# Kernel tuning notes

Hardware: AMD Instinct MI355X
Metric: run time of the kernel (lower is better)

## Reference

```python
import jax, jax.numpy as jnp
import numpy as np

HEADS = 8
D_MODEL = 512
HEAD_DIM = D_MODEL // HEADS


def setup_inputs() -> dict:
    key = jax.random.key(0)
    ks = jax.random.split(key, 13)
    B, S, D = 8, 1024, D_MODEL
    scale = 1.0 / np.sqrt(D)
    x = jax.random.normal(ks[0], (B, S, D), dtype=jnp.float32)
    names = ['cq', 'ck', 'cv', 'pq', 'pk', 'pv']
    inp = {'x': x}
    for i, n in enumerate(names):
        inp['W_' + n] = jax.random.normal(ks[1 + 2 * i], (D, D), dtype=jnp.float32) * scale
        inp['b_' + n] = jax.random.normal(ks[2 + 2 * i], (D,), dtype=jnp.float32) * 0.01
    return inp


def reference(x, W_cq, b_cq, W_ck, b_ck, W_cv, b_cv, W_pq, b_pq, W_pk, b_pk, W_pv, b_pv):
    # x: [N, S, D]. Fused common + personal QKV: (x@Wc + bc) + (x@Wp + bp)
    N, S, D = x.shape
    q = x @ (W_cq + W_pq) + (b_cq + b_pq)  # [N, S, D]
    k = x @ (W_ck + W_pk) + (b_ck + b_pk)
    v = x @ (W_cv + W_pv) + (b_cv + b_pv)
    q = q.reshape(N, S, HEADS, HEAD_DIM)
    k = k.reshape(N, S, HEADS, HEAD_DIM)
    v = v.reshape(N, S, HEADS, HEAD_DIM)
    # NOTE: original scales by sqrt(d_model), not sqrt(head_dim)
    energy = jnp.einsum('nqhd,nkhd->nhqk', q, k) / jnp.sqrt(jnp.asarray(D, x.dtype))
    attn = jax.nn.softmax(energy, axis=-1)  # [N, H, Q, K]
    out = jnp.einsum('nhqk,nkhd->nqhd', attn, v).reshape(N, S, D)
    return out
```

## Files before the change

### kernel.cpp

```cpp
#include <hip/hip_runtime.h>

#define B_   8
#define S_   1024
#define D_   512
#define H_   8
#define HD_  64
#define NT_  (B_ * S_)
#define QSCALE_ 0.06376387f
#define C4_    5.7707802f

typedef _Float16 f16;
typedef _Float16 f16x4 __attribute__((ext_vector_type(4)));
typedef _Float16 f16x8 __attribute__((ext_vector_type(8)));
typedef float    f32x4 __attribute__((ext_vector_type(4)));

#define GLOAD_LDS16(g, l) \
    __builtin_amdgcn_global_load_lds( \
        (const __attribute__((address_space(1))) unsigned int*)(g), \
        (__attribute__((address_space(3))) unsigned int*)(l), 16, 0, 0)

#define MFMA16(a, b, c) __builtin_amdgcn_mfma_f32_16x16x32_f16(a, b, c, 0, 0, 0)

__global__ __launch_bounds__(256) void prep_fused(
    const float* __restrict__ x, f16* __restrict__ xh,
    const float* __restrict__ Wcq, const float* __restrict__ Wck, const float* __restrict__ Wcv,
    const float* __restrict__ Wpq, const float* __restrict__ Wpk, const float* __restrict__ Wpv,
    f16* __restrict__ Bt)
{
    __shared__ float tile[64][68];
    const int tid = threadIdx.x;

    if (blockIdx.x < 2048) {
        int i = (blockIdx.x * 256 + tid) * 8;
        float4 a = *(const float4*)(x + i);
        float4 b = *(const float4*)(x + i + 4);
        f16x8 o = { (f16)a.x, (f16)a.y, (f16)a.z, (f16)a.w,
                    (f16)b.x, (f16)b.y, (f16)b.z, (f16)b.w };
        *(f16x8*)(xh + i) = o;
        return;
    }

    const int wk = blockIdx.x - 2048;
    const int k0 = (wk & 7) * 64;
    const int n0 = (wk >> 3) * 64;
    const int g  = n0 >> 9;
    const int c0 = n0 & 511;
    const float* Wc = (g == 0) ? Wcq : (g == 1) ? Wck : Wcv;
    const float* Wp = (g == 0) ? Wpq : (g == 1) ? Wpk : Wpv;

#pragma unroll
    for (int it = 0; it < 4; ++it) {
        int row = it * 16 + (tid >> 4);
        int c4  = (tid & 15) * 4;
        float4 a = *(const float4*)(Wc + (size_t)(k0 + row) * D_ + c0 + c4);
        float4 b = *(const float4*)(Wp + (size_t)(k0 + row) * D_ + c0 + c4);
        tile[row][c4 + 0] = a.x + b.x;
        tile[row][c4 + 1] = a.y + b.y;
        tile[row][c4 + 2] = a.z + b.z;
        tile[row][c4 + 3] = a.w + b.w;
    }
    __syncthreads();
#pragma unroll
    for (int it = 0; it < 2; ++it) {
        int nr = it * 32 + (tid >> 3);
        int kc = (tid & 7) * 8;
        f16x8 o;
#pragma unroll
        for (int j = 0; j < 8; ++j) o[j] = (f16)tile[kc + j][nr];
        *(f16x8*)(Bt + (size_t)(n0 + nr) * D_ + k0 + kc) = o;
    }
}

__global__ __launch_bounds__(256) void qkv_gemm(
    const f16* __restrict__ xh, const f16* __restrict__ Bt,
    const float* __restrict__ bcq, const float* __restrict__ bck, const float* __restrict__ bcv,
    const float* __restrict__ bpq, const float* __restrict__ bpk, const float* __restrict__ bpv,
    f16* __restrict__ Qh, f16* __restrict__ Kws, f16* __restrict__ Vws)
{
    __shared__ __align__(16) char smem_raw[36864];

    const int m0 = blockIdx.x * 128;
    const int n0 = blockIdx.y * 128;
    const int tid  = threadIdx.x;
    const int lane = tid & 63;
    const int wave = tid >> 6;
    const int wr = wave >> 1, wc = wave & 1;
    const int lo4 = lane & 15, hi4 = lane >> 4;

    const int r0 = tid >> 2;
    const int w0 = tid & 3;
    const f16* gA  = xh + (size_t)(m0 + r0) * D_ + w0 * 8;
    const f16* gA2 = xh + (size_t)(m0 + r0 + 64) * D_ + w0 * 8;
    const f16* gB  = Bt + (size_t)(n0 + r0) * D_ + w0 * 8;
    const f16* gB2 = Bt + (size_t)(n0 + r0 + 64) * D_ + w0 * 8;
    const int dA  = tid * 8;
    const int dA2 = (tid + 256) * 8;

#define STAGE(bufsel, kt) do { \
        f16* _A = (f16*)(smem_raw + (bufsel) * 16384); \
        f16* _B = (f16*)(smem_raw + (bufsel) * 16384 + 8192); \
        GLOAD_LDS16(gA  + (kt) * 32, _A + dA);  \
        GLOAD_LDS16(gA2 + (kt) * 32, _A + dA2); \
        GLOAD_LDS16(gB  + (kt) * 32, _B + dA);  \
        GLOAD_LDS16(gB2 + (kt) * 32, _B + dA2); \
    } while (0)

    f32x4 acc[4][4];
#pragma unroll
    for (int i = 0; i < 4; ++i)
#pragma unroll
        for (int j = 0; j < 4; ++j) acc[i][j] = (f32x4){0.f, 0.f, 0.f, 0.f};

    STAGE(0, 0);
    asm volatile("s_waitcnt vmcnt(0)" ::: "memory");
    __syncthreads();

    for (int t = 0; t < 16; ++t) {
        const int cur = t & 1;
        if (t < 15) STAGE(cur ^ 1, t + 1);

        const f16* Ab = (const f16*)(smem_raw + cur * 16384);
        const f16* Bb = (const f16*)(smem_raw + cur * 16384 + 8192);
        f16x8 a[4], b[4];
#pragma unroll
        for (int i = 0; i < 4; ++i)
            a[i] = *(const f16x8*)(Ab + (wr * 64 + i * 16 + lo4) * 32 + hi4 * 8);
#pragma unroll
        for (int j = 0; j < 4; ++j)
            b[j] = *(const f16x8*)(Bb + (wc * 64 + j * 16 + lo4) * 32 + hi4 * 8);
#pragma unroll
        for (int i = 0; i < 4; ++i)
#pragma unroll
            for (int j = 0; j < 4; ++j)
                acc[i][j] = MFMA16(a[i], b[j], acc[i][j]);

        asm volatile("s_waitcnt vmcnt(0)" ::: "memory");
        __syncthreads();
    }
#undef STAGE

    const int g = n0 >> 9;
    const float* bc = (g == 0) ? bcq : (g == 1) ? bck : bcv;
    const float* bp = (g == 0) ? bpq : (g == 1) ? bpk : bpv;

    const int colb = n0 + wc * 64;
    const int h    = (colb & 511) >> 6;
    const int rowb = m0 + wr * 64;
    const int bb   = rowb >> 10;
    const int s0   = rowb & 1023;

    float bias[4];
#pragma unroll
    for (int j = 0; j < 4; ++j) {
        const int cg = (colb + j * 16 + lo4) & 511;
        bias[j] = bc[cg] + bp[cg];
    }

    f16* Cs = (f16*)smem_raw + wave * 4608;
    const size_t bhbase = (size_t)(bb * H_ + h) * 65536;

    if (g == 2) {
#pragma unroll
        for (int i = 0; i < 4; ++i)
#pragma unroll
            for (int j = 0; j < 4; ++j) {
                f16x4 v = { (f16)(acc[i][j][0] + bias[j]), (f16)(acc[i][j][1] + bias[j]),
                            (f16)(acc[i][j][2] + bias[j]), (f16)(acc[i][j][3] + bias[j]) };
                *(f16x4*)(Cs + (j * 16 + lo4) * 72 + i * 16 + hi4 * 4) = v;
            }
        asm volatile("s_waitcnt lgkmcnt(0)" ::: "memory");
        __builtin_amdgcn_sched_barrier(0);
        const size_t tbase = bhbase + (size_t)(s0 >> 6) * 4096;
#pragma unroll
        for (int it = 0; it < 8; ++it) {
            const int d  = it * 8 + (lane >> 3);
            const int cs = lane & 7;
            f16x8 chunk = *(const f16x8*)(Cs + d * 72 + cs * 8);
            *(f16x8*)(Vws + tbase + d * 64 + ((cs ^ (d & 7)) << 3)) = chunk;
        }
    } else {
        const float scale = (g == 0) ? QSCALE_ : 1.f;
#pragma unroll
        for (int i = 0; i < 4; ++i)
#pragma unroll
            for (int j = 0; j < 4; ++j)
#pragma unroll
                for (int r = 0; r < 4; ++r)
                    Cs[(i * 16 + hi4 * 4 + r) * 72 + j * 16 + lo4] =
                        (f16)((acc[i][j][r] + bias[j]) * scale);
        asm volatile("s_waitcnt lgkmcnt(0)" ::: "memory");
        __builtin_amdgcn_sched_barrier(0);
#pragma unroll
        for (int it = 0; it < 8; ++it) {
            const int rr = it * 8 + (lane >> 3);
            const int ci = lane & 7;
            f16x8 chunk = *(const f16x8*)(Cs + rr * 72 + ci * 8);
            if (g == 0) {
                *(f16x8*)(Qh + bhbase + (size_t)(s0 + rr) * 64 + ci * 8) = chunk;
            } else {
                const size_t tbase = bhbase + (size_t)(s0 >> 6) * 4096;
                *(f16x8*)(Kws + tbase + rr * 64 + ((ci ^ (rr & 7)) << 3)) = chunk;
            }
        }
    }
}

__global__ __launch_bounds__(256) void attn_fwd(
    const f16* __restrict__ Qh, const f16* __restrict__ Kws,
    const f16* __restrict__ Vws, float* __restrict__ out)
{
    __shared__ __align__(16) f16 Ks[2][4096];
    __shared__ __align__(16) f16 Vs[2][4096];
    __shared__ __align__(16) f16 Ps[4][32 * 72];

    const int b0 = blockIdx.x;
    const int bh = (b0 & 7) * 8 + ((b0 >> 3) & 7);
    const int qt = b0 >> 6;

    const int wave = threadIdx.x >> 6;
    const int lane = threadIdx.x & 63;
    const int lo4 = lane & 15, hi4 = lane >> 4;
    const int q0 = qt * 128 + wave * 32;

    const f16* Qp = Qh  + (size_t)bh * 65536;
    const f16* Kp = Kws + (size_t)bh * 65536;
    const f16* Vp = Vws + (size_t)bh * 65536;
    f16* Pw = &Ps[wave][0];

    f16x8 aq[2][2];
#pragma unroll
    for (int qg = 0; qg < 2; ++qg)
#pragma unroll
        for (int hh = 0; hh < 2; ++hh)
            aq[qg][hh] = *(const f16x8*)(Qp + (q0 + qg * 16 + lo4) * 64 + hh * 32 + hi4 * 8);

    f32x4 o[2][4];
    float l[2][4];
#pragma unroll
    for (int qg = 0; qg < 2; ++qg)
#pragma unroll
        for (int dt = 0; dt < 4; ++dt) {
            o[qg][dt] = (f32x4){0.f, 0.f, 0.f, 0.f};
            l[qg][dt] = 0.f;
        }

    const int soff = threadIdx.x * 8;
    GLOAD_LDS16(Kp + soff,        &Ks[0][soff]);
    GLOAD_LDS16(Kp + 2048 + soff, &Ks[0][2048 + soff]);
    GLOAD_LDS16(Vp + soff,        &Vs[0][soff]);
    GLOAD_LDS16(Vp + 2048 + soff, &Vs[0][2048 + soff]);
    asm volatile("s_waitcnt vmcnt(0)" ::: "memory");
    __syncthreads();

    for (int t = 0; t < 16; ++t) {
        const int cur = t & 1;
        if (t < 15) {
            const f16* Kn = Kp + (t + 1) * 4096;
            const f16* Vn = Vp + (t + 1) * 4096;
            GLOAD_LDS16(Kn + soff,        &Ks[cur ^ 1][soff]);
            GLOAD_LDS16(Kn + 2048 + soff, &Ks[cur ^ 1][2048 + soff]);
            GLOAD_LDS16(Vn + soff,        &Vs[cur ^ 1][soff]);
            GLOAD_LDS16(Vn + 2048 + soff, &Vs[cur ^ 1][2048 + soff]);
        }
        const f16* Kc = &Ks[cur][0];
        const f16* Vc = &Vs[cur][0];

#pragma unroll
        for (int f = 0; f < 4; ++f) {
            const int c = f * 16 + lo4;
            f16x8 bk0 = *(const f16x8*)(Kc + c * 64 + ((hi4 ^ (c & 7)) << 3));
            f16x8 bk1 = *(const f16x8*)(Kc + c * 64 + (((4 + hi4) ^ (c & 7)) << 3));
#pragma unroll
            for (int qg = 0; qg < 2; ++qg) {
                f32x4 sc = (f32x4){0.f, 0.f, 0.f, 0.f};
                sc = MFMA16(aq[qg][0], bk0, sc);
                sc = MFMA16(aq[qg][1], bk1, sc);
#pragma unroll
                for (int r = 0; r < 4; ++r) {
                    float p = __builtin_amdgcn_exp2f(sc[r] - C4_);
                    l[qg][r] += p;
                    Pw[(qg * 16 + hi4 * 4 + r) * 72 + f * 16 + lo4] = (f16)p;
                }
            }
        }
        asm volatile("s_waitcnt lgkmcnt(0)" ::: "memory");
        __builtin_amdgcn_sched_barrier(0);

        f16x8 ap[2][2];
#pragma unroll
        for (int qg = 0; qg < 2; ++qg) {
            ap[qg][0] = *(const f16x8*)(Pw + (qg * 16 + lo4) * 72 + hi4 * 8);
            ap[qg][1] = *(const f16x8*)(Pw + (qg * 16 + lo4) * 72 + 32 + hi4 * 8);
        }
#pragma unroll
        for (int dt = 0; dt < 4; ++dt) {
            const int d = dt * 16 + lo4;
            f16x8 bv0 = *(const f16x8*)(Vc + d * 64 + ((hi4 ^ (d & 7)) << 3));
            f16x8 bv1 = *(const f16x8*)(Vc + d * 64 + (((4 + hi4) ^ (d & 7)) << 3));
#pragma unroll
            for (int qg = 0; qg < 2; ++qg) {
                o[qg][dt] = MFMA16(ap[qg][0], bv0, o[qg][dt]);
                o[qg][dt] = MFMA16(ap[qg][1], bv1, o[qg][dt]);
            }
        }

        asm volatile("s_waitcnt vmcnt(0)" ::: "memory");
        __syncthreads();
    }

    const int b = bh >> 3;
    const int h = bh & 7;
#pragma unroll
    for (int qg = 0; qg < 2; ++qg)
#pragma unroll
        for (int r = 0; r < 4; ++r) {
            float lv = l[qg][r];
            lv += __shfl_xor(lv, 1);
            lv += __shfl_xor(lv, 2);
            lv += __shfl_xor(lv, 4);
            lv += __shfl_xor(lv, 8);
            const float inv = 1.f / lv;
            const int s_idx = q0 + qg * 16 + hi4 * 4 + r;
            float* op = out + ((size_t)(b * S_ + s_idx)) * D_ + h * HD_;
#pragma unroll
            for (int dt = 0; dt < 4; ++dt)
                op[dt * 16 + lo4] = o[qg][dt][r] * inv;
        }
}

extern "C" void kernel_launch(void* const* d_in, const int* in_sizes, int n_in,
                              void* d_out, int out_size, void* d_ws, size_t ws_size,
                              hipStream_t stream)
{
    const float* x   = (const float*)d_in[0];
    const float* Wcq = (const float*)d_in[1];
    const float* bcq = (const float*)d_in[2];
    const float* Wck = (const float*)d_in[3];
    const float* bck = (const float*)d_in[4];
    const float* Wcv = (const float*)d_in[5];
    const float* bcv = (const float*)d_in[6];
    const float* Wpq = (const float*)d_in[7];
    const float* bpq = (const float*)d_in[8];
    const float* Wpk = (const float*)d_in[9];
    const float* bpk = (const float*)d_in[10];
    const float* Wpv = (const float*)d_in[11];
    const float* bpv = (const float*)d_in[12];

    f16* ws = (f16*)d_ws;
    f16* xh  = ws;
    f16* Bt  = xh + (size_t)NT_ * D_;
    f16* Qh  = Bt + (size_t)3 * D_ * D_;
    f16* Kws = Qh + (size_t)64 * 65536;
    f16* Vws = Kws + (size_t)64 * 65536;
    float* o = (float*)d_out;

    prep_fused<<<2240, 256, 0, stream>>>(x, xh, Wcq, Wck, Wcv, Wpq, Wpk, Wpv, Bt);
    qkv_gemm<<<dim3(64, 12), 256, 0, stream>>>(xh, Bt, bcq, bck, bcv, bpq, bpk, bpv,
                                               Qh, Kws, Vws);
    attn_fwd<<<512, 256, 0, stream>>>(Qh, Kws, Vws, o);
}
```

Before: 60.57 us.

## Pre-tile GEMM operands into contiguous k-slab blocks and remap blocks per XCD

The prep kernel now writes x and the fused weights in a tiled layout, where each 128-row by 32-k slab is contiguous and column-chunk-major. The GEMM can then load each stage with fully contiguous global-to-LDS copies, and its LDS reads become conflict-free 16-byte strided accesses. The GEMM grid is also flattened, and block IDs are remapped so that each XCD handles a contiguous group of M tiles, which is meant to improve L2 reuse. In exchange, the prep kernel's x conversion does strided row reads, and both kernels now depend on the new layout matching exactly.

New measurement: 58.02 us. -4.2%, faster.

```diff
diff --git a/kernel.cpp b/kernel.cpp
--- a/kernel.cpp
+++ b/kernel.cpp
@@ -21,26 +21,36 @@
 
 #define MFMA16(a, b, c) __builtin_amdgcn_mfma_f32_16x16x32_f16(a, b, c, 0, 0, 0)
 
+
 __global__ __launch_bounds__(256) void prep_fused(
-    const float* __restrict__ x, f16* __restrict__ xh,
+    const float* __restrict__ x, f16* __restrict__ xh_t,
     const float* __restrict__ Wcq, const float* __restrict__ Wck, const float* __restrict__ Wcv,
     const float* __restrict__ Wpq, const float* __restrict__ Wpk, const float* __restrict__ Wpv,
-    f16* __restrict__ Bt)
+    f16* __restrict__ Bt_t)
 {
     __shared__ float tile[64][68];
     const int tid = threadIdx.x;
 
-    if (blockIdx.x < 2048) {
-        int i = (blockIdx.x * 256 + tid) * 8;
-        float4 a = *(const float4*)(x + i);
-        float4 b = *(const float4*)(x + i + 4);
-        f16x8 o = { (f16)a.x, (f16)a.y, (f16)a.z, (f16)a.w,
-                    (f16)b.x, (f16)b.y, (f16)b.z, (f16)b.w };
-        *(f16x8*)(xh + i) = o;
+    if (blockIdx.x < 1024) {
+        const int mtile = blockIdx.x >> 4;
+        const int ktile = blockIdx.x & 15;
+        f16* dst = xh_t + ((size_t)mtile * 16 + ktile) * 4096;
+#pragma unroll
+        for (int half = 0; half < 2; ++half) {
+            const int q = half * 256 + tid;
+            const int r = q >> 2;
+            const int c = q & 3;
+            const float* src = x + (size_t)(mtile * 128 + r) * D_ + ktile * 32 + c * 8;
+            float4 a = *(const float4*)(src);
+            float4 b = *(const float4*)(src + 4);
+            f16x8 o = { (f16)a.x, (f16)a.y, (f16)a.z, (f16)a.w,
+                        (f16)b.x, (f16)b.y, (f16)b.z, (f16)b.w };
+            *(f16x8*)(dst + c * 1024 + r * 8) = o;
+        }
         return;
     }
 
-    const int wk = blockIdx.x - 2048;
+    const int wk = blockIdx.x - 1024;
     const int k0 = (wk & 7) * 64;
     const int n0 = (wk >> 3) * 64;
     const int g  = n0 >> 9;
@@ -60,6 +70,9 @@
         tile[row][c4 + 3] = a.w + b.w;
     }
     __syncthreads();
+
+    const int ntile = n0 >> 7;
+    const int rbase = n0 & 64;
 #pragma unroll
     for (int it = 0; it < 2; ++it) {
         int nr = it * 32 + (tid >> 3);
@@ -67,42 +80,45 @@
         f16x8 o;
 #pragma unroll
         for (int j = 0; j < 8; ++j) o[j] = (f16)tile[kc + j][nr];
-        *(f16x8*)(Bt + (size_t)(n0 + nr) * D_ + k0 + kc) = o;
+        const int kt = (k0 + kc) >> 5;
+        const int c  = (kc >> 3) & 3;
+        const int r  = rbase + nr;
+        *(f16x8*)(Bt_t + ((size_t)ntile * 16 + kt) * 4096 + c * 1024 + r * 8) = o;
     }
 }
 
 __global__ __launch_bounds__(256) void qkv_gemm(
-    const f16* __restrict__ xh, const f16* __restrict__ Bt,
+    const f16* __restrict__ xh_t, const f16* __restrict__ Bt_t,
     const float* __restrict__ bcq, const float* __restrict__ bck, const float* __restrict__ bcv,
     const float* __restrict__ bpq, const float* __restrict__ bpk, const float* __restrict__ bpv,
     f16* __restrict__ Qh, f16* __restrict__ Kws, f16* __restrict__ Vws)
 {
     __shared__ __align__(16) char smem_raw[36864];
 
-    const int m0 = blockIdx.x * 128;
-    const int n0 = blockIdx.y * 128;
+    const int bid   = blockIdx.x;
+    const int xcd   = bid & 7;
+    const int idx   = bid >> 3;
+    const int mtile = xcd * 8 + (idx & 7);
+    const int ntile = idx >> 3;
+    const int m0 = mtile * 128;
+    const int n0 = ntile * 128;
+
     const int tid  = threadIdx.x;
     const int lane = tid & 63;
     const int wave = tid >> 6;
     const int wr = wave >> 1, wc = wave & 1;
     const int lo4 = lane & 15, hi4 = lane >> 4;
 
-    const int r0 = tid >> 2;
-    const int w0 = tid & 3;
-    const f16* gA  = xh + (size_t)(m0 + r0) * D_ + w0 * 8;
-    const f16* gA2 = xh + (size_t)(m0 + r0 + 64) * D_ + w0 * 8;
-    const f16* gB  = Bt + (size_t)(n0 + r0) * D_ + w0 * 8;
-    const f16* gB2 = Bt + (size_t)(n0 + r0 + 64) * D_ + w0 * 8;
-    const int dA  = tid * 8;
-    const int dA2 = (tid + 256) * 8;
+    const f16* gA = xh_t + (size_t)mtile * 16 * 4096;
+    const f16* gB = Bt_t + (size_t)ntile * 16 * 4096;
 
 #define STAGE(bufsel, kt) do { \
         f16* _A = (f16*)(smem_raw + (bufsel) * 16384); \
         f16* _B = (f16*)(smem_raw + (bufsel) * 16384 + 8192); \
-        GLOAD_LDS16(gA  + (kt) * 32, _A + dA);  \
-        GLOAD_LDS16(gA2 + (kt) * 32, _A + dA2); \
-        GLOAD_LDS16(gB  + (kt) * 32, _B + dA);  \
-        GLOAD_LDS16(gB2 + (kt) * 32, _B + dA2); \
+        GLOAD_LDS16(gA + (kt) * 4096 + tid * 8,         _A + tid * 8);         \
+        GLOAD_LDS16(gA + (kt) * 4096 + (tid + 256) * 8, _A + (tid + 256) * 8); \
+        GLOAD_LDS16(gB + (kt) * 4096 + tid * 8,         _B + tid * 8);         \
+        GLOAD_LDS16(gB + (kt) * 4096 + (tid + 256) * 8, _B + (tid + 256) * 8); \
     } while (0)
 
     f32x4 acc[4][4];
@@ -124,10 +140,10 @@
         f16x8 a[4], b[4];
 #pragma unroll
         for (int i = 0; i < 4; ++i)
-            a[i] = *(const f16x8*)(Ab + (wr * 64 + i * 16 + lo4) * 32 + hi4 * 8);
+            a[i] = *(const f16x8*)(Ab + hi4 * 1024 + (wr * 64 + i * 16 + lo4) * 8);
 #pragma unroll
         for (int j = 0; j < 4; ++j)
-            b[j] = *(const f16x8*)(Bb + (wc * 64 + j * 16 + lo4) * 32 + hi4 * 8);
+            b[j] = *(const f16x8*)(Bb + hi4 * 1024 + (wc * 64 + j * 16 + lo4) * 8);
 #pragma unroll
         for (int i = 0; i < 4; ++i)
 #pragma unroll
@@ -347,15 +363,15 @@
     const float* bpv = (const float*)d_in[12];
 
     f16* ws = (f16*)d_ws;
-    f16* xh  = ws;
-    f16* Bt  = xh + (size_t)NT_ * D_;
-    f16* Qh  = Bt + (size_t)3 * D_ * D_;
-    f16* Kws = Qh + (size_t)64 * 65536;
-    f16* Vws = Kws + (size_t)64 * 65536;
+    f16* xh_t = ws;
+    f16* Bt_t = xh_t + (size_t)64 * 16 * 4096;
+    f16* Qh   = Bt_t + (size_t)12 * 16 * 4096;
+    f16* Kws  = Qh + (size_t)64 * 65536;
+    f16* Vws  = Kws + (size_t)64 * 65536;
     float* o = (float*)d_out;
 
-    prep_fused<<<2240, 256, 0, stream>>>(x, xh, Wcq, Wck, Wcv, Wpq, Wpk, Wpv, Bt);
-    qkv_gemm<<<dim3(64, 12), 256, 0, stream>>>(xh, Bt, bcq, bck, bcv, bpq, bpk, bpv,
-                                               Qh, Kws, Vws);
+    prep_fused<<<1216, 256, 0, stream>>>(x, xh_t, Wcq, Wck, Wcv, Wpq, Wpk, Wpv, Bt_t);
+    qkv_gemm<<<768, 256, 0, stream>>>(xh_t, Bt_t, bcq, bck, bcv, bpq, bpk, bpv,
+                                      Qh, Kws, Vws);
     attn_fwd<<<512, 256, 0, stream>>>(Qh, Kws, Vws, o);
 }
```
